# Kernel optimization log

Hardware: AMD Instinct MI355X
Metric: run time of the kernel (lower is better)

The kernel has to match this reference:

```python
import jax, jax.numpy as jnp
import numpy as np

CUTOFF = 5.0
N_ENV = 8
F0, F1 = 16, 32  # filter_dims
D = 256          # feature_dim


def setup_inputs() -> dict:
    key = jax.random.key(0)
    ks = jax.random.split(key, 12)
    B, E, N = 128, 64, 32
    r = jax.random.normal(ks[0], (B, E, 3), jnp.float32) * 3.0
    # neighbors placed near r so distances fall inside the cutoff
    r_nb = r[..., None, :] + jax.random.normal(ks[1], (B, E, N, 3), jnp.float32) * 1.5
    ee_scales = jax.random.uniform(ks[2], (N_ENV,), jnp.float32, 0.5, CUTOFF)
    ee_kernel = jax.random.normal(ks[3], (4, F0), jnp.float32) / jnp.sqrt(4.0)
    ee_bias = jax.random.normal(ks[4], (F0,), jnp.float32) * 2.0
    beta_kernel = jax.random.normal(ks[5], (F0 + N_ENV, F1), jnp.float32) / jnp.sqrt(F0 + N_ENV + 0.0)
    beta_bias = jnp.zeros((F1,), jnp.float32)
    gamma_kernel = jax.random.normal(ks[6], (F1, D), jnp.float32) / jnp.sqrt(F1 + 0.0)
    dense1_kernel = jax.random.normal(ks[7], (4, D), jnp.float32) / jnp.sqrt(4.0)
    dense1_bias = jnp.zeros((D,), jnp.float32)
    out_kernel = jax.random.normal(ks[8], (D, D), jnp.float32) / jnp.sqrt(D + 0.0)
    out_bias = jnp.zeros((D,), jnp.float32)
    return dict(r=r, r_nb=r_nb, ee_scales=ee_scales, ee_kernel=ee_kernel, ee_bias=ee_bias,
                beta_kernel=beta_kernel, beta_bias=beta_bias, gamma_kernel=gamma_kernel,
                dense1_kernel=dense1_kernel, dense1_bias=dense1_bias,
                out_kernel=out_kernel, out_bias=out_bias)


def reference(r, r_nb, ee_scales, ee_kernel, ee_bias, beta_kernel, beta_bias,
              gamma_kernel, dense1_kernel, dense1_bias, out_kernel, out_bias):
    # pairwise diff features: [dist, dx, dy, dz] per neighbor
    diff = r_nb - r[..., None, :]                       # [B,E,N,3]
    dist = jnp.linalg.norm(diff, axis=-1, keepdims=True)  # [B,E,N,1]
    feats = jnp.concatenate([dist, diff], axis=-1)      # [B,E,N,4]

    # PairwiseFilter (beta_ee): envelopes + small dense, gated by smooth cutoff
    env = jnp.exp(-jnp.square(dist / ee_scales))        # [B,E,N,N_ENV]
    h = jnp.tanh(feats @ ee_kernel + ee_bias)           # [B,E,N,F0]
    x = dist / CUTOFF
    fcut = jnp.where(x < 1.0, 0.5 * (jnp.cos(jnp.pi * x) + 1.0), 0.0)
    beta = (jnp.concatenate([h, env], axis=-1) @ beta_kernel + beta_bias) * fcut  # [B,E,N,F1]

    gamma = beta @ gamma_kernel                         # [B,E,N,D]

    # rescale features: first column (dist) becomes log1p(dist)
    inp = feats / dist * jnp.log1p(dist)                # [B,E,N,4]
    feat = jax.nn.silu(inp @ dense1_kernel + dense1_bias)  # [B,E,N,D]

    res = jnp.einsum('...id,...id->...d', feat, gamma)  # sum over neighbors -> [B,E,D]
    res = jax.nn.silu(res @ out_kernel + out_bias)
    return res
```

## Files before the change

### kernel.cpp

```cpp
#include <hip/hip_runtime.h>
#include <hip/hip_bf16.h>

constexpr int NB   = 32;
constexpr int NENV = 8;
constexpr int F0   = 16;
constexpr int F1   = 32;
constexpr int D    = 256;
constexpr int PAIRS = 128 * 64;
constexpr float CUT = 5.0f;

typedef float f32x4 __attribute__((ext_vector_type(4)));
typedef short s16x8 __attribute__((ext_vector_type(8)));

__device__ __forceinline__ float fast_rcp(float x) { return __builtin_amdgcn_rcpf(x); }
__device__ __forceinline__ float silu(float a) {
  return a * fast_rcp(1.0f + __expf(-a));
}
__device__ __forceinline__ float fast_tanh(float t) {
  return 1.0f - 2.0f * fast_rcp(__expf(2.0f * t) + 1.0f);
}
__device__ __forceinline__ unsigned int cvt_pk_bf16(float a, float b) {
  unsigned int r;
  asm("v_cvt_pk_bf16_f32 %0, %1, %2" : "=v"(r) : "v"(a), "v"(b));
  return r;
}
__device__ __forceinline__ unsigned short f2bf(float f) {
  return (unsigned short)(cvt_pk_bf16(f, f) & 0xffffu);
}

__global__ __launch_bounds__(256)
__attribute__((amdgpu_waves_per_eu(4, 4)))
void moon_fused(
    const float* __restrict__ r,
    const float* __restrict__ r_nb,
    const float* __restrict__ ee_scales,
    const float* __restrict__ ee_kernel,
    const float* __restrict__ ee_bias,
    const float* __restrict__ beta_kernel,
    const float* __restrict__ beta_bias,
    const float* __restrict__ gamma_kernel,
    const float* __restrict__ dense1_kernel,
    const float* __restrict__ dense1_bias,
    const float* __restrict__ out_kernel,
    const float* __restrict__ out_bias,
    float* __restrict__ out)
{
  __shared__ float s_eek[4 * F0];
  __shared__ float s_eeb[F0];
  __shared__ float s_is2[NENV];
  __shared__ unsigned short s_ghT[4][D * 8];
  __shared__ unsigned short s_d1kT[D * 8];
  __shared__ unsigned short s_bkh[4][F1 * 8];
  __shared__ unsigned short s_hb[4][4][NB * 8];
  __shared__ unsigned short s_inph[4][NB * 8];
  __shared__ float s_fcut[4][NB];
  __shared__ unsigned short s_resall[4 * 264];

  const int tid = threadIdx.x;
  const int w   = tid >> 6;
  const int l   = tid & 63;
  const int be  = blockIdx.x * 4 + w;
  const int be0 = blockIdx.x * 4;

  if (tid < 64)       s_eek[tid]      = ee_kernel[tid];
  else if (tid < 80)  s_eeb[tid - 64] = ee_bias[tid - 64];
  else if (tid < 88) { float s = ee_scales[tid - 80]; s_is2[tid - 80] = 1.0f / (s * s); }

  if (tid < 128) {
    const int c = tid & 31;
    const int g = tid >> 5;
    unsigned int q[4];
    if (g < 3) {
      float v[8];
      #pragma unroll
      for (int j = 0; j < 8; ++j) v[j] = beta_kernel[(g * 8 + j) * F1 + c];
      q[0] = cvt_pk_bf16(v[0], v[1]); q[1] = cvt_pk_bf16(v[2], v[3]);
      q[2] = cvt_pk_bf16(v[4], v[5]); q[3] = cvt_pk_bf16(v[6], v[7]);
    } else {
      q[0] = cvt_pk_bf16(beta_bias[c], 0.0f); q[1] = 0; q[2] = 0; q[3] = 0;
    }
    *(uint4*)&s_bkh[g][c * 8] = make_uint4(q[0], q[1], q[2], q[3]);
  }

  {
    const int d = tid;
    unsigned int pk[16];
    #pragma unroll
    for (int k2 = 0; k2 < 16; ++k2)
      pk[k2] = cvt_pk_bf16(gamma_kernel[(2 * k2 + 0) * D + d],
                           gamma_kernel[(2 * k2 + 1) * D + d]);
    #pragma unroll
    for (int g = 0; g < 4; ++g)
      *(uint4*)&s_ghT[g][d * 8] = make_uint4(pk[4*g], pk[4*g+1], pk[4*g+2], pk[4*g+3]);
  }
  {
    const int d = tid;
    unsigned int p0 = cvt_pk_bf16(0.25f * dense1_kernel[0 * D + d],
                                  0.25f * dense1_kernel[1 * D + d]);
    unsigned int p1 = cvt_pk_bf16(0.25f * dense1_kernel[2 * D + d],
                                  0.25f * dense1_kernel[3 * D + d]);
    unsigned int p2 = cvt_pk_bf16(0.25f * dense1_bias[d], 0.0f);
    *(uint4*)&s_d1kT[d * 8] = make_uint4(p0, p1, p2, 0u);
  }

  __syncthreads();

  const int li = l & 15;
  const int g  = l >> 4;

  {
    const int n    = l & 31;
    const int half = l >> 5;
    float rx = r[be * 3 + 0];
    float ry = r[be * 3 + 1];
    float rz = r[be * 3 + 2];
    const float* rn = r_nb + (be * NB + n) * 3;
    float dx = rn[0] - rx;
    float dy = rn[1] - ry;
    float dz = rn[2] - rz;
    float d2 = dx * dx + dy * dy + dz * dz;
    float dist = sqrtf(d2);
    float feats[4] = {dist, dx, dy, dz};
    float h[8];
    #pragma unroll
    for (int j8 = 0; j8 < 8; ++j8) {
      int j = half * 8 + j8;
      float t = s_eeb[j];
      #pragma unroll
      for (int i = 0; i < 4; ++i) t += feats[i] * s_eek[i * F0 + j];
      h[j8] = fast_tanh(t);
    }
    unsigned int hp0 = cvt_pk_bf16(h[0], h[1]);
    unsigned int hp1 = cvt_pk_bf16(h[2], h[3]);
    unsigned int hp2 = cvt_pk_bf16(h[4], h[5]);
    unsigned int hp3 = cvt_pk_bf16(h[6], h[7]);
    if (half == 0) {
      *(uint4*)&s_hb[w][0][n * 8] = make_uint4(hp0, hp1, hp2, hp3);
      *(uint4*)&s_hb[w][3][n * 8] = make_uint4(0x3F80u, 0u, 0u, 0u);
      float lp  = log1pf(dist);
      float inv = lp / dist;
      unsigned int q0 = cvt_pk_bf16(lp, dx * inv);
      unsigned int q1 = cvt_pk_bf16(dy * inv, dz * inv);
      *(uint4*)&s_inph[w][n * 8] = make_uint4(q0, q1, 0x3F80u, 0u);
    } else {
      *(uint4*)&s_hb[w][1][n * 8] = make_uint4(hp0, hp1, hp2, hp3);
      float env[NENV];
      #pragma unroll
      for (int s = 0; s < NENV; ++s) env[s] = __expf(-d2 * s_is2[s]);
      unsigned int e0 = cvt_pk_bf16(env[0], env[1]);
      unsigned int e1 = cvt_pk_bf16(env[2], env[3]);
      unsigned int e2 = cvt_pk_bf16(env[4], env[5]);
      unsigned int e3 = cvt_pk_bf16(env[6], env[7]);
      *(uint4*)&s_hb[w][2][n * 8] = make_uint4(e0, e1, e2, e3);
      float xc = dist * (1.0f / CUT);
      s_fcut[w][n] = (xc < 1.0f)
                   ? 0.5f * (__cosf(3.14159265358979323846f * xc) + 1.0f)
                   : 0.0f;
    }
  }

  {
    s16x8 ah0 = *(const s16x8*)&s_hb[w][g][(0 * 16 + li) * 8];
    s16x8 ah1 = *(const s16x8*)&s_hb[w][g][(1 * 16 + li) * 8];
    s16x8 bb0 = *(const s16x8*)&s_bkh[g][(0 * 16 + li) * 8];
    s16x8 bb1 = *(const s16x8*)&s_bkh[g][(1 * 16 + li) * 8];
    f32x4 z = {0.f, 0.f, 0.f, 0.f};
    f32x4 c00 = __builtin_amdgcn_mfma_f32_16x16x32_bf16(ah0, bb0, z, 0, 0, 0);
    f32x4 c01 = __builtin_amdgcn_mfma_f32_16x16x32_bf16(ah0, bb1, z, 0, 0, 0);
    f32x4 c10 = __builtin_amdgcn_mfma_f32_16x16x32_bf16(ah1, bb0, z, 0, 0, 0);
    f32x4 c11 = __builtin_amdgcn_mfma_f32_16x16x32_bf16(ah1, bb1, z, 0, 0, 0);
    const int cl = li >> 3;
    const int sl = li & 7;
    #pragma unroll
    for (int reg = 0; reg < 4; ++reg) {
      int row0 = g * 4 + reg;
      int row1 = 16 + g * 4 + reg;
      float fc0 = s_fcut[w][row0];
      float fc1 = s_fcut[w][row1];
      s_hb[w][cl    ][row0 * 8 + sl] = f2bf(c00[reg] * fc0);
      s_hb[w][2 + cl][row0 * 8 + sl] = f2bf(c01[reg] * fc0);
      s_hb[w][cl    ][row1 * 8 + sl] = f2bf(c10[reg] * fc1);
      s_hb[w][2 + cl][row1 * 8 + sl] = f2bf(c11[reg] * fc1);
    }
  }

  {
    s16x8 a0 = *(const s16x8*)&s_hb[w][g][(0 * 16 + li) * 8];
    s16x8 a1 = *(const s16x8*)&s_hb[w][g][(1 * 16 + li) * 8];
    s16x8 ai0 = *(const s16x8*)&s_inph[w][(0 * 16 + li) * 8];
    s16x8 ai1 = *(const s16x8*)&s_inph[w][(1 * 16 + li) * 8];

    #pragma unroll 4
    for (int nt = 0; nt < 16; ++nt) {
      const int d = nt * 16 + li;
      s16x8 b  = *(const s16x8*)&s_ghT[g][d * 8];
      s16x8 bd = *(const s16x8*)&s_d1kT[d * 8];
      f32x4 z = {0.f, 0.f, 0.f, 0.f};
      f32x4 c0 = __builtin_amdgcn_mfma_f32_16x16x32_bf16(a0, b, z, 0, 0, 0);
      f32x4 c1 = __builtin_amdgcn_mfma_f32_16x16x32_bf16(a1, b, z, 0, 0, 0);
      f32x4 f0 = __builtin_amdgcn_mfma_f32_16x16x32_bf16(ai0, bd, z, 0, 0, 0);
      f32x4 f1 = __builtin_amdgcn_mfma_f32_16x16x32_bf16(ai1, bd, z, 0, 0, 0);
      float pv = 0.f;
      #pragma unroll
      for (int reg = 0; reg < 4; ++reg) {
        pv += silu(f0[reg]) * c0[reg];
        pv += silu(f1[reg]) * c1[reg];
      }
      pv += __shfl_xor(pv, 16);
      pv += __shfl_xor(pv, 32);
      if (g == (nt & 3)) s_resall[w * 264 + nt * 16 + li] = f2bf(pv);
    }
  }
  __syncthreads();

  {
    const int col0 = w * 64;
    float bi[4];
    #pragma unroll
    for (int nt = 0; nt < 4; ++nt) bi[nt] = out_bias[col0 + nt * 16 + li];

    f32x4 acc[4] = {{0.f,0.f,0.f,0.f},{0.f,0.f,0.f,0.f},{0.f,0.f,0.f,0.f},{0.f,0.f,0.f,0.f}};
    const unsigned short* arow = &s_resall[(li & 3) * 264 + g * 8];
    const float* wp = out_kernel + col0 + li;

    #pragma unroll 2
    for (int ks = 0; ks < 8; ++ks) {
      s16x8 a = *(const s16x8*)(arow + ks * 32);
      const float* wk0 = wp + (ks * 32 + g * 8) * D;
      #pragma unroll
      for (int nt = 0; nt < 4; ++nt) {
        const float* wq = wk0 + nt * 16;
        union { s16x8 v; unsigned int u[4]; } ub;
        #pragma unroll
        for (int jj = 0; jj < 4; ++jj)
          ub.u[jj] = cvt_pk_bf16(wq[(2 * jj) * D], wq[(2 * jj + 1) * D]);
        acc[nt] = __builtin_amdgcn_mfma_f32_16x16x32_bf16(a, ub.v, acc[nt], 0, 0, 0);
      }
    }
    if (g == 0) {
      #pragma unroll
      for (int nt = 0; nt < 4; ++nt) {
        #pragma unroll
        for (int reg = 0; reg < 4; ++reg) {
          out[(be0 + reg) * D + col0 + nt * 16 + li] = silu(acc[nt][reg] + bi[nt]);
        }
      }
    }
  }
}

extern "C" void kernel_launch(void* const* d_in, const int* in_sizes, int n_in,
                              void* d_out, int out_size, void* d_ws, size_t ws_size,
                              hipStream_t stream) {
  const float* r            = (const float*)d_in[0];
  const float* r_nb         = (const float*)d_in[1];
  const float* ee_scales    = (const float*)d_in[2];
  const float* ee_kernel    = (const float*)d_in[3];
  const float* ee_bias      = (const float*)d_in[4];
  const float* beta_kernel  = (const float*)d_in[5];
  const float* beta_bias    = (const float*)d_in[6];
  const float* gamma_kernel = (const float*)d_in[7];
  const float* dense1_kernel= (const float*)d_in[8];
  const float* dense1_bias  = (const float*)d_in[9];
  const float* out_kernel   = (const float*)d_in[10];
  const float* out_bias     = (const float*)d_in[11];
  float* out = (float*)d_out;

  hipLaunchKernelGGL(moon_fused, dim3(PAIRS / 4), dim3(256), 0, stream,
                     r, r_nb, ee_scales, ee_kernel, ee_bias,
                     beta_kernel, beta_bias, gamma_kernel,
                     dense1_kernel, dense1_bias, out_kernel, out_bias, out);
}
```

Before: 113.8 us.

## Process eight pairs per block to amortize weight staging and output GEMM

Each block now handles eight (batch, electron) pairs instead of four. Each wave processes two pairs, and each lane computes all features for one neighbor of one pair. This halves the number of blocks, so the per-block shared-memory weight staging and the out_kernel global loads feeding the final MFMA happen half as often, and the M=16 MFMA tile now has 8 real rows instead of 4. In exchange there is more per-wave serial work and more shared memory, and the waves_per_eu occupancy hint is dropped, which may change register allocation and occupancy.

```diff
diff --git a/kernel.cpp b/kernel.cpp
--- a/kernel.cpp
+++ b/kernel.cpp
@@ -29,7 +29,6 @@
 }
 
 __global__ __launch_bounds__(256)
-__attribute__((amdgpu_waves_per_eu(4, 4)))
 void moon_fused(
     const float* __restrict__ r,
     const float* __restrict__ r_nb,
@@ -51,16 +50,15 @@
   __shared__ unsigned short s_ghT[4][D * 8];
   __shared__ unsigned short s_d1kT[D * 8];
   __shared__ unsigned short s_bkh[4][F1 * 8];
-  __shared__ unsigned short s_hb[4][4][NB * 8];
-  __shared__ unsigned short s_inph[4][NB * 8];
-  __shared__ float s_fcut[4][NB];
-  __shared__ unsigned short s_resall[4 * 264];
+  __shared__ unsigned short s_hb[8][4][NB * 8];
+  __shared__ unsigned short s_inph[8][NB * 8];
+  __shared__ float s_fcut[8][NB];
+  __shared__ unsigned short s_resall[8 * 264];
 
   const int tid = threadIdx.x;
   const int w   = tid >> 6;
   const int l   = tid & 63;
-  const int be  = blockIdx.x * 4 + w;
-  const int be0 = blockIdx.x * 4;
+  const int be0 = blockIdx.x * 8;
 
   if (tid < 64)       s_eek[tid]      = ee_kernel[tid];
   else if (tid < 80)  s_eeb[tid - 64] = ee_bias[tid - 64];
@@ -109,59 +107,61 @@
   const int g  = l >> 4;
 
   {
-    const int n    = l & 31;
-    const int half = l >> 5;
-    float rx = r[be * 3 + 0];
-    float ry = r[be * 3 + 1];
-    float rz = r[be * 3 + 2];
-    const float* rn = r_nb + (be * NB + n) * 3;
+    const int ph = l >> 5;
+    const int n  = l & 31;
+    const int p  = w * 2 + ph;
+    const int bep = be0 + p;
+    float rx = r[bep * 3 + 0];
+    float ry = r[bep * 3 + 1];
+    float rz = r[bep * 3 + 2];
+    const float* rn = r_nb + (bep * NB + n) * 3;
     float dx = rn[0] - rx;
     float dy = rn[1] - ry;
     float dz = rn[2] - rz;
     float d2 = dx * dx + dy * dy + dz * dz;
     float dist = sqrtf(d2);
     float feats[4] = {dist, dx, dy, dz};
-    float h[8];
-    #pragma unroll
-    for (int j8 = 0; j8 < 8; ++j8) {
-      int j = half * 8 + j8;
+    float h[16];
+    #pragma unroll
+    for (int j = 0; j < 16; ++j) {
       float t = s_eeb[j];
       #pragma unroll
       for (int i = 0; i < 4; ++i) t += feats[i] * s_eek[i * F0 + j];
-      h[j8] = fast_tanh(t);
+      h[j] = fast_tanh(t);
     }
     unsigned int hp0 = cvt_pk_bf16(h[0], h[1]);
     unsigned int hp1 = cvt_pk_bf16(h[2], h[3]);
     unsigned int hp2 = cvt_pk_bf16(h[4], h[5]);
     unsigned int hp3 = cvt_pk_bf16(h[6], h[7]);
-    if (half == 0) {
-      *(uint4*)&s_hb[w][0][n * 8] = make_uint4(hp0, hp1, hp2, hp3);
-      *(uint4*)&s_hb[w][3][n * 8] = make_uint4(0x3F80u, 0u, 0u, 0u);
-      float lp  = log1pf(dist);
-      float inv = lp / dist;
-      unsigned int q0 = cvt_pk_bf16(lp, dx * inv);
-      unsigned int q1 = cvt_pk_bf16(dy * inv, dz * inv);
-      *(uint4*)&s_inph[w][n * 8] = make_uint4(q0, q1, 0x3F80u, 0u);
-    } else {
-      *(uint4*)&s_hb[w][1][n * 8] = make_uint4(hp0, hp1, hp2, hp3);
-      float env[NENV];
-      #pragma unroll
-      for (int s = 0; s < NENV; ++s) env[s] = __expf(-d2 * s_is2[s]);
-      unsigned int e0 = cvt_pk_bf16(env[0], env[1]);
-      unsigned int e1 = cvt_pk_bf16(env[2], env[3]);
-      unsigned int e2 = cvt_pk_bf16(env[4], env[5]);
-      unsigned int e3 = cvt_pk_bf16(env[6], env[7]);
-      *(uint4*)&s_hb[w][2][n * 8] = make_uint4(e0, e1, e2, e3);
-      float xc = dist * (1.0f / CUT);
-      s_fcut[w][n] = (xc < 1.0f)
-                   ? 0.5f * (__cosf(3.14159265358979323846f * xc) + 1.0f)
-                   : 0.0f;
-    }
-  }
-
-  {
-    s16x8 ah0 = *(const s16x8*)&s_hb[w][g][(0 * 16 + li) * 8];
-    s16x8 ah1 = *(const s16x8*)&s_hb[w][g][(1 * 16 + li) * 8];
+    unsigned int hp4 = cvt_pk_bf16(h[8], h[9]);
+    unsigned int hp5 = cvt_pk_bf16(h[10], h[11]);
+    unsigned int hp6 = cvt_pk_bf16(h[12], h[13]);
+    unsigned int hp7 = cvt_pk_bf16(h[14], h[15]);
+    *(uint4*)&s_hb[p][0][n * 8] = make_uint4(hp0, hp1, hp2, hp3);
+    *(uint4*)&s_hb[p][1][n * 8] = make_uint4(hp4, hp5, hp6, hp7);
+    *(uint4*)&s_hb[p][3][n * 8] = make_uint4(0x3F80u, 0u, 0u, 0u);
+    float env[NENV];
+    #pragma unroll
+    for (int s = 0; s < NENV; ++s) env[s] = __expf(-d2 * s_is2[s]);
+    unsigned int e0 = cvt_pk_bf16(env[0], env[1]);
+    unsigned int e1 = cvt_pk_bf16(env[2], env[3]);
+    unsigned int e2 = cvt_pk_bf16(env[4], env[5]);
+    unsigned int e3 = cvt_pk_bf16(env[6], env[7]);
+    *(uint4*)&s_hb[p][2][n * 8] = make_uint4(e0, e1, e2, e3);
+    float lp  = log1pf(dist);
+    float inv = lp / dist;
+    unsigned int q0 = cvt_pk_bf16(lp, dx * inv);
+    unsigned int q1 = cvt_pk_bf16(dy * inv, dz * inv);
+    *(uint4*)&s_inph[p][n * 8] = make_uint4(q0, q1, 0x3F80u, 0u);
+    float xc = dist * (1.0f / CUT);
+    s_fcut[p][n] = (xc < 1.0f)
+                 ? 0.5f * (__cosf(3.14159265358979323846f * xc) + 1.0f)
+                 : 0.0f;
+  }
+
+  auto beta_pair = [&](int p) {
+    s16x8 ah0 = *(const s16x8*)&s_hb[p][g][(0 * 16 + li) * 8];
+    s16x8 ah1 = *(const s16x8*)&s_hb[p][g][(1 * 16 + li) * 8];
     s16x8 bb0 = *(const s16x8*)&s_bkh[g][(0 * 16 + li) * 8];
     s16x8 bb1 = *(const s16x8*)&s_bkh[g][(1 * 16 + li) * 8];
     f32x4 z = {0.f, 0.f, 0.f, 0.f};
@@ -175,20 +175,22 @@
     for (int reg = 0; reg < 4; ++reg) {
       int row0 = g * 4 + reg;
       int row1 = 16 + g * 4 + reg;
-      float fc0 = s_fcut[w][row0];
-      float fc1 = s_fcut[w][row1];
-      s_hb[w][cl    ][row0 * 8 + sl] = f2bf(c00[reg] * fc0);
-      s_hb[w][2 + cl][row0 * 8 + sl] = f2bf(c01[reg] * fc0);
-      s_hb[w][cl    ][row1 * 8 + sl] = f2bf(c10[reg] * fc1);
-      s_hb[w][2 + cl][row1 * 8 + sl] = f2bf(c11[reg] * fc1);
-    }
-  }
-
-  {
-    s16x8 a0 = *(const s16x8*)&s_hb[w][g][(0 * 16 + li) * 8];
-    s16x8 a1 = *(const s16x8*)&s_hb[w][g][(1 * 16 + li) * 8];
-    s16x8 ai0 = *(const s16x8*)&s_inph[w][(0 * 16 + li) * 8];
-    s16x8 ai1 = *(const s16x8*)&s_inph[w][(1 * 16 + li) * 8];
+      float fc0 = s_fcut[p][row0];
+      float fc1 = s_fcut[p][row1];
+      s_hb[p][cl    ][row0 * 8 + sl] = f2bf(c00[reg] * fc0);
+      s_hb[p][2 + cl][row0 * 8 + sl] = f2bf(c01[reg] * fc0);
+      s_hb[p][cl    ][row1 * 8 + sl] = f2bf(c10[reg] * fc1);
+      s_hb[p][2 + cl][row1 * 8 + sl] = f2bf(c11[reg] * fc1);
+    }
+  };
+  beta_pair(w * 2 + 0);
+  beta_pair(w * 2 + 1);
+
+  auto phase2_pair = [&](int p) {
+    s16x8 a0 = *(const s16x8*)&s_hb[p][g][(0 * 16 + li) * 8];
+    s16x8 a1 = *(const s16x8*)&s_hb[p][g][(1 * 16 + li) * 8];
+    s16x8 ai0 = *(const s16x8*)&s_inph[p][(0 * 16 + li) * 8];
+    s16x8 ai1 = *(const s16x8*)&s_inph[p][(1 * 16 + li) * 8];
 
     #pragma unroll 4
     for (int nt = 0; nt < 16; ++nt) {
@@ -208,9 +210,12 @@
       }
       pv += __shfl_xor(pv, 16);
       pv += __shfl_xor(pv, 32);
-      if (g == (nt & 3)) s_resall[w * 264 + nt * 16 + li] = f2bf(pv);
-    }
-  }
+      if (g == (nt & 3)) s_resall[p * 264 + nt * 16 + li] = f2bf(pv);
+    }
+  };
+  phase2_pair(w * 2 + 0);
+  phase2_pair(w * 2 + 1);
+
   __syncthreads();
 
   {
@@ -220,7 +225,7 @@
     for (int nt = 0; nt < 4; ++nt) bi[nt] = out_bias[col0 + nt * 16 + li];
 
     f32x4 acc[4] = {{0.f,0.f,0.f,0.f},{0.f,0.f,0.f,0.f},{0.f,0.f,0.f,0.f},{0.f,0.f,0.f,0.f}};
-    const unsigned short* arow = &s_resall[(li & 3) * 264 + g * 8];
+    const unsigned short* arow = &s_resall[(li & 7) * 264 + g * 8];
     const float* wp = out_kernel + col0 + li;
 
     #pragma unroll 2
@@ -237,12 +242,12 @@
         acc[nt] = __builtin_amdgcn_mfma_f32_16x16x32_bf16(a, ub.v, acc[nt], 0, 0, 0);
       }
     }
-    if (g == 0) {
+    if (g < 2) {
       #pragma unroll
       for (int nt = 0; nt < 4; ++nt) {
         #pragma unroll
         for (int reg = 0; reg < 4; ++reg) {
-          out[(be0 + reg) * D + col0 + nt * 16 + li] = silu(acc[nt][reg] + bi[nt]);
+          out[(be0 + g * 4 + reg) * D + col0 + nt * 16 + li] = silu(acc[nt][reg] + bi[nt]);
         }
       }
     }
@@ -265,8 +270,9 @@
   const float* out_kernel   = (const float*)d_in[10];
   const float* out_bias     = (const float*)d_in[11];
   float* out = (float*)d_out;
-
-  hipLaunchKernelGGL(moon_fused, dim3(PAIRS / 4), dim3(256), 0, stream,
+  (void)d_ws; (void)ws_size;
+
+  hipLaunchKernelGGL(moon_fused, dim3(PAIRS / 8), dim3(256), 0, stream,
                      r, r_nb, ee_scales, ee_kernel, ee_bias,
                      beta_kernel, beta_bias, gamma_kernel,
                      dense1_kernel, dense1_bias, out_kernel, out_bias, out);
```

After: 115.5 us. Within noise of the previous version (+1.5%).
